# Performance work log

Hardware: AMD Instinct MI355X
Metric: run time of the kernel (lower is better)

The kernel has to match this reference:

```python
import jax, jax.numpy as jnp
import numpy as np

N = 50000        # nodes
E = 200000       # edges
D_IN = 128       # dim_input
D_E = 32         # dim_edge_features
D_H = 256        # dim_hidden
D_OUT = 256      # dim_output
N_LAYERS = 3
N_FRAG = 10000
N_GRAPH = 2000
BN_EPS = 1e-5
GINE_EPS = 0.0   # eps buffer, train_eps=False

_LAYER_DIMS = [(D_IN, D_H), (D_H, D_H), (D_H, D_OUT)]  # (node in, node out) per layer


def setup_inputs() -> dict:
    key = jax.random.key(0)
    ks = iter(jax.random.split(key, 64))
    inp = {}
    inp['x'] = jax.random.normal(next(ks), (N, D_IN), dtype=jnp.float32)
    inp['edge_attr'] = jax.random.normal(next(ks), (E, D_E), dtype=jnp.float32)
    inp['edge_index'] = jax.random.randint(next(ks), (2, E), 0, N, dtype=jnp.int64)
    inp['frag_batch'] = jnp.sort(jax.random.randint(next(ks), (N,), 0, N_FRAG, dtype=jnp.int64))
    inp['graph_batch'] = jnp.sort(jax.random.randint(next(ks), (N,), 0, N_GRAPH, dtype=jnp.int64))
    for i, (din, dout) in enumerate(_LAYER_DIMS):
        fin = din + D_E  # MLP input = node feat + edge feat (post-concat message)
        inp[f'w1_{i}'] = jax.random.normal(next(ks), (fin, D_H), dtype=jnp.float32) / np.sqrt(fin)
        inp[f'b1_{i}'] = jnp.zeros((D_H,), dtype=jnp.float32)
        inp[f'w2_{i}'] = jax.random.normal(next(ks), (D_H, dout), dtype=jnp.float32) / np.sqrt(D_H)
        inp[f'b2_{i}'] = jnp.zeros((dout,), dtype=jnp.float32)
        inp[f'g_{i}'] = jnp.ones((dout,), dtype=jnp.float32)     # BN weight
        inp[f'beta_{i}'] = jnp.zeros((dout,), dtype=jnp.float32)  # BN bias
    return inp


def _gine_layer(x, edge_attr, src, dst, w1, b1, w2, b2, g, beta):
    # message: relu(concat(x_j, e_ji)) gathered along edges  -> [E, din+De]
    m = jax.nn.relu(jnp.concatenate([x[src], edge_attr], axis=-1))
    # aggregate: scatter-add into target nodes -> [N, din+De]
    agg = jax.ops.segment_sum(m, dst, num_segments=N)
    # (1+eps)*x residual on the node-feature slice
    agg = agg.at[:, : x.shape[1]].add((1.0 + GINE_EPS) * x)
    # h_Theta MLP: Linear -> ReLU -> Linear
    h = jnp.dot(jax.nn.relu(jnp.dot(agg, w1) + b1), w2) + b2
    # ReLU then BatchNorm1d(track_running_stats=False): batch stats, biased var
    h = jax.nn.relu(h)
    mu = h.mean(axis=0)
    var = h.var(axis=0)
    return g * (h - mu) * jax.lax.rsqrt(var + BN_EPS) + beta


def _sqrt_pool(h, batch, num_segments):
    # nodes_per_graph, broadcast back per-node, sqrt-normalize, then add-pool
    cnt = jax.ops.segment_sum(jnp.ones((h.shape[0],), h.dtype), batch, num_segments=num_segments)
    inv_sqrt = jax.lax.rsqrt(jnp.maximum(cnt, 1.0))[batch]  # [N]
    return jax.ops.segment_sum(h * inv_sqrt[:, None], batch, num_segments=num_segments)


def reference(x, edge_attr, edge_index, frag_batch, graph_batch,
              w1_0, b1_0, w2_0, b2_0, g_0, beta_0,
              w1_1, b1_1, w2_1, b2_1, g_1, beta_1,
              w1_2, b1_2, w2_2, b2_2, g_2, beta_2):
    src, dst = edge_index[0], edge_index[1]
    params = [(w1_0, b1_0, w2_0, b2_0, g_0, beta_0),
              (w1_1, b1_1, w2_1, b2_1, g_1, beta_1),
              (w1_2, b1_2, w2_2, b2_2, g_2, beta_2)]
    h = x
    for p in params:
        h = _gine_layer(h, edge_attr, src, dst, *p)
    frag_out = _sqrt_pool(h, frag_batch, N_FRAG)    # [N_FRAG, D_OUT]
    graph_out = _sqrt_pool(h, graph_batch, N_GRAPH)  # [N_GRAPH, D_OUT]
    return (frag_out, graph_out)
```

## Files before the change

kernel.cpp:

```cpp
#include <hip/hip_runtime.h>

#define N_NODES 50000
#define N_EDGES 200000
#define DE 32
#define N_FRAG 10000
#define N_GRAPH 2000
#define BN_SLOTS 32
#define KSTR 296

typedef _Float16 f16x8 __attribute__((ext_vector_type(8)));
typedef _Float16 f16x4 __attribute__((ext_vector_type(4)));
typedef __attribute__((ext_vector_type(4))) float f32x4;

__device__ __forceinline__ float4 ld4(const float* p) { return *(const float4*)p; }
__device__ __forceinline__ float4 ld4(const _Float16* p) {
    f16x4 h = *(const f16x4*)p;
    float4 v; v.x = (float)h[0]; v.y = (float)h[1]; v.z = (float)h[2]; v.w = (float)h[3];
    return v;
}
__device__ __forceinline__ void st4h(_Float16* p, float4 v) {
    f16x4 h = {(_Float16)v.x, (_Float16)v.y, (_Float16)v.z, (_Float16)v.w};
    *(f16x4*)p = h;
}

__global__ __launch_bounds__(256)
void block_sum_kernel(const int* __restrict__ deg, int* __restrict__ bsum) {
    int i = blockIdx.x * 256 + threadIdx.x;
    int v = (i < N_NODES) ? deg[i] : 0;
#pragma unroll
    for (int o = 1; o < 64; o <<= 1) v += __shfl_xor(v, o);
    __shared__ int wsum[4];
    if ((threadIdx.x & 63) == 0) wsum[threadIdx.x >> 6] = v;
    __syncthreads();
    if (threadIdx.x == 0) bsum[blockIdx.x] = wsum[0] + wsum[1] + wsum[2] + wsum[3];
}

__global__ __launch_bounds__(256)
void top_scan_kernel(int* __restrict__ bsum, int nb) {
    __shared__ int s[256];
    int t = threadIdx.x;
    s[t] = (t < nb) ? bsum[t] : 0;
    __syncthreads();
    for (int o = 1; o < 256; o <<= 1) {
        int v = s[t];
        int a = (t >= o) ? s[t - o] : 0;
        __syncthreads();
        s[t] = v + a;
        __syncthreads();
    }
    if (t < nb) bsum[t] = (t > 0) ? s[t - 1] : 0;
}

__global__ __launch_bounds__(256)
void final_scan_kernel(const int* __restrict__ deg, const int* __restrict__ bsum,
                       int* __restrict__ ptr) {
    __shared__ int s[256];
    int i = blockIdx.x * 256 + threadIdx.x;
    int t = threadIdx.x;
    int v = (i < N_NODES) ? deg[i] : 0;
    s[t] = v;
    __syncthreads();
    for (int o = 1; o < 256; o <<= 1) {
        int x = s[t];
        int a = (t >= o) ? s[t - o] : 0;
        __syncthreads();
        s[t] = x + a;
        __syncthreads();
    }
    int incl = s[t];
    int base = bsum[blockIdx.x];
    if (i < N_NODES) ptr[i] = base + incl - v;
    if (i == N_NODES - 1) ptr[N_NODES] = base + incl;
}

__global__ __launch_bounds__(256)
void fill_csr_kernel(const int* __restrict__ ei, const int* __restrict__ row_ptr,
                     int* __restrict__ fill, int* __restrict__ csr_src,
                     int* __restrict__ csr_eid) {
    int e = blockIdx.x * 256 + threadIdx.x;
    if (e >= N_EDGES) return;
    int dst = ei[N_EDGES + e];
    int pos = row_ptr[dst] + atomicAdd(&fill[dst], 1);
    csr_src[pos] = ei[e];
    csr_eid[pos] = e;
}

struct PrepArgs {
    const float* W[6];
    _Float16* BS[6];
    int base[7];
    int nb_bs;
    const int* ei;
    int* deg;
    int nb_deg;
    const int* fb; const int* gb;
    int* frag_ptr; int* graph_ptr;
    int nb_seg;
    const float* x;
    _Float16* y0;
};

__global__ __launch_bounds__(256)
void prep1_kernel(PrepArgs a) {
    int b = blockIdx.x;
    const int t = threadIdx.x;
    if (b < a.nb_bs) {
        int id = b * 256 + t;
        if (id < a.base[6]) {
            int seg = 0;
#pragma unroll
            for (int i = 1; i < 6; ++i) seg += (id >= a.base[i]);
            int lid = id - a.base[seg];
            int j  = lid & 7;
            int l  = (lid >> 3) & 63;
            int cg = (lid >> 9) & 15;
            int kt = lid >> 13;
            int col = cg * 16 + (l & 15);
            int k   = kt * 32 + (l >> 4) * 8 + j;
            a.BS[seg][lid] = (_Float16)a.W[seg][(size_t)k * 256 + col];
        }
        return;
    }
    b -= a.nb_bs;
    if (b < a.nb_deg) {
        int e = b * 256 + t;
        if (e < N_EDGES) atomicAdd(&a.deg[a.ei[N_EDGES + e]], 1);
        return;
    }
    b -= a.nb_deg;
    if (b < a.nb_seg) {
        int id = b * 256 + t;
        const int* batch;
        int* ptr;
        int s;
        if (id <= N_FRAG) { batch = a.fb; ptr = a.frag_ptr; s = id; }
        else if (id <= N_FRAG + 1 + N_GRAPH) { batch = a.gb; ptr = a.graph_ptr; s = id - (N_FRAG + 1); }
        else return;
        int lo = 0, hi = N_NODES;
        while (lo < hi) {
            int mid = (lo + hi) >> 1;
            if (batch[mid] < s) lo = mid + 1; else hi = mid;
        }
        ptr[s] = lo;
        return;
    }
    b -= a.nb_seg;
    size_t i = ((size_t)b * 256 + t) * 4;
    if (i < (size_t)N_NODES * 128) {
        float4 v = ld4(a.x + i);
        f16x4 o = {(_Float16)fmaxf(v.x, 0.f), (_Float16)fmaxf(v.y, 0.f),
                   (_Float16)fmaxf(v.z, 0.f), (_Float16)fmaxf(v.w, 0.f)};
        *(f16x4*)(a.y0 + i) = o;
    }
}

__global__ __launch_bounds__(256)
void bnfin_relu16_kernel(const float* __restrict__ slots,
                         const float* __restrict__ g, const float* __restrict__ beta,
                         const _Float16* __restrict__ h, _Float16* __restrict__ y,
                         float* __restrict__ scale_out, float* __restrict__ shift_out) {
    __shared__ float ssc[256], ssh[256];
    const int t = threadIdx.x;
    {
        float s = 0.f, q = 0.f;
        for (int k = 0; k < BN_SLOTS; ++k) {
            s += slots[(size_t)k * 512 + t];
            q += slots[(size_t)k * 512 + 256 + t];
        }
        float mu = s * (1.0f / N_NODES);
        float var = q * (1.0f / N_NODES) - mu * mu;
        float rstd = rsqrtf(var + 1e-5f);
        float sc = g[t] * rstd;
        float sh = beta[t] - mu * sc;
        ssc[t] = sc; ssh[t] = sh;
        if (blockIdx.x == 0) { scale_out[t] = sc; shift_out[t] = sh; }
    }
    __syncthreads();
    const size_t total = (size_t)N_NODES * 256 / 8;
    for (size_t idx = (size_t)blockIdx.x * 256 + t; idx < total;
         idx += (size_t)gridDim.x * 256) {
        size_t i = idx * 8;
        int col = (int)(i & 255);
        f16x8 v = *(const f16x8*)(h + i);
        f16x8 o;
#pragma unroll
        for (int k2 = 0; k2 < 8; ++k2)
            o[k2] = (_Float16)fmaxf(fmaf((float)v[k2], ssc[col + k2], ssh[col + k2]), 0.f);
        *(f16x8*)(y + i) = o;
    }
}

template <bool BNIN, typename T, int NC>
__global__ __launch_bounds__(512, 4)
void fused_mlp_kernel(const T* __restrict__ X, const _Float16* __restrict__ Yg,
                      const int* __restrict__ row_ptr, const int* __restrict__ csr_src,
                      const int* __restrict__ csr_eid, const float* __restrict__ ea,
                      float* __restrict__ agg_e,
                      const float* __restrict__ bnsc, const float* __restrict__ bnsh,
                      const _Float16* __restrict__ B1, const float* __restrict__ bias1,
                      const _Float16* __restrict__ B2, const float* __restrict__ bias2,
                      _Float16* __restrict__ C, float* __restrict__ bnslot) {
    constexpr int DIN  = NC * 32;
    constexpr int K1   = DIN + 32;
    constexpr int NKT1 = K1 / 32;
    constexpr int CPT  = DIN / 8;
    constexpr int NV   = CPT / 8;
    __shared__ __align__(16) _Float16 sBuf[64 * KSTR];
    const int t = threadIdx.x;
    const int l = t & 63;
    const int w = t >> 6;
    const int lr = l & 15;
    const int lq = l >> 4;
    const int row0 = blockIdx.x << 6;
    const int cb = w << 5;

    {
        const int r = t >> 3, j = t & 7;
        const int jc = j << 3;
        const int gr = row0 + r;
        if (gr < N_NODES) {
            f16x8 acc16[NV];
#pragma unroll
            for (int c = 0; c < NV; ++c) acc16[c] = (f16x8){0, 0, 0, 0, 0, 0, 0, 0};
            float4 eacc = {0.f, 0.f, 0.f, 0.f};
            const int beg = row_ptr[gr], end = row_ptr[gr + 1];
            for (int e = beg; e < end; ++e) {
                const _Float16* sp = Yg + (size_t)csr_src[e] * DIN + jc;
#pragma unroll
                for (int c = 0; c < NV; ++c) acc16[c] += *(const f16x8*)(sp + c * 64);
                if (!BNIN) {
                    float4 ev = *(const float4*)(ea + (size_t)csr_eid[e] * DE + (j << 2));
                    eacc.x += fmaxf(ev.x, 0.f);
                    eacc.y += fmaxf(ev.y, 0.f);
                    eacc.z += fmaxf(ev.z, 0.f);
                    eacc.w += fmaxf(ev.w, 0.f);
                }
            }
            const T* xp = X + (size_t)gr * DIN + jc;
#pragma unroll
            for (int c = 0; c < NV; ++c) {
                float4 v0f = ld4(xp + c * 64);
                float4 v1f = ld4(xp + c * 64 + 4);
                if (BNIN) {
                    float4 sa = *(const float4*)(bnsc + c * 64 + jc);
                    float4 sb = *(const float4*)(bnsc + c * 64 + jc + 4);
                    float4 ta = *(const float4*)(bnsh + c * 64 + jc);
                    float4 tb = *(const float4*)(bnsh + c * 64 + jc + 4);
                    v0f.x = fmaf(v0f.x, sa.x, ta.x);
                    v0f.y = fmaf(v0f.y, sa.y, ta.y);
                    v0f.z = fmaf(v0f.z, sa.z, ta.z);
                    v0f.w = fmaf(v0f.w, sa.w, ta.w);
                    v1f.x = fmaf(v1f.x, sb.x, tb.x);
                    v1f.y = fmaf(v1f.y, sb.y, tb.y);
                    v1f.z = fmaf(v1f.z, sb.z, tb.z);
                    v1f.w = fmaf(v1f.w, sb.w, tb.w);
                }
                f16x8 o;
                o[0] = (_Float16)(v0f.x + (float)acc16[c][0]);
                o[1] = (_Float16)(v0f.y + (float)acc16[c][1]);
                o[2] = (_Float16)(v0f.z + (float)acc16[c][2]);
                o[3] = (_Float16)(v0f.w + (float)acc16[c][3]);
                o[4] = (_Float16)(v1f.x + (float)acc16[c][4]);
                o[5] = (_Float16)(v1f.y + (float)acc16[c][5]);
                o[6] = (_Float16)(v1f.z + (float)acc16[c][6]);
                o[7] = (_Float16)(v1f.w + (float)acc16[c][7]);
                *(f16x8*)&sBuf[r * KSTR + c * 64 + jc] = o;
            }
            if (!BNIN) {
                *(float4*)(agg_e + (size_t)gr * DE + (j << 2)) = eacc;
                st4h(&sBuf[r * KSTR + DIN + (j << 2)], eacc);
            } else {
                float4 ev = *(const float4*)(agg_e + (size_t)gr * DE + (j << 2));
                st4h(&sBuf[r * KSTR + DIN + (j << 2)], ev);
            }
        } else {
            f16x8 z8 = {0, 0, 0, 0, 0, 0, 0, 0};
#pragma unroll
            for (int c = 0; c < NV; ++c)
                *(f16x8*)&sBuf[r * KSTR + c * 64 + jc] = z8;
            f16x4 z4 = {0, 0, 0, 0};
            *(f16x4*)&sBuf[r * KSTR + DIN + (j << 2)] = z4;
        }
    }
    __syncthreads();

    f32x4 acc1[4][2];
#pragma unroll
    for (int mt = 0; mt < 4; ++mt)
#pragma unroll
        for (int nt = 0; nt < 2; ++nt) acc1[mt][nt] = (f32x4){0.f, 0.f, 0.f, 0.f};
#pragma unroll
    for (int kt = 0; kt < NKT1; ++kt) {
        f16x8 af[4], bf[2];
#pragma unroll
        for (int mt = 0; mt < 4; ++mt)
            af[mt] = *(const f16x8*)&sBuf[(mt * 16 + lr) * KSTR + (kt << 5) + (lq << 3)];
        const size_t bb = ((size_t)(kt * 16 + (w << 1))) * 512 + (l << 3);
#pragma unroll
        for (int nt = 0; nt < 2; ++nt)
            bf[nt] = *(const f16x8*)(B1 + bb + nt * 512);
#pragma unroll
        for (int mt = 0; mt < 4; ++mt)
#pragma unroll
            for (int nt = 0; nt < 2; ++nt)
                acc1[mt][nt] = __builtin_amdgcn_mfma_f32_16x16x32_f16(
                    af[mt], bf[nt], acc1[mt][nt], 0, 0, 0);
    }
    __syncthreads();

#pragma unroll
    for (int nt = 0; nt < 2; ++nt) {
        int col = cb + nt * 16 + lr;
        float bv = bias1[col];
#pragma unroll
        for (int mt = 0; mt < 4; ++mt)
#pragma unroll
            for (int i = 0; i < 4; ++i) {
                int rr = mt * 16 + lq * 4 + i;
                sBuf[rr * KSTR + col] = (_Float16)fmaxf(acc1[mt][nt][i] + bv, 0.f);
            }
    }
    __syncthreads();

    f32x4 acc2[4][2];
#pragma unroll
    for (int mt = 0; mt < 4; ++mt)
#pragma unroll
        for (int nt = 0; nt < 2; ++nt) acc2[mt][nt] = (f32x4){0.f, 0.f, 0.f, 0.f};
#pragma unroll
    for (int kt = 0; kt < 8; ++kt) {
        f16x8 af[4], bf[2];
#pragma unroll
        for (int mt = 0; mt < 4; ++mt)
            af[mt] = *(const f16x8*)&sBuf[(mt * 16 + lr) * KSTR + (kt << 5) + (lq << 3)];
        const size_t bb = ((size_t)(kt * 16 + (w << 1))) * 512 + (l << 3);
#pragma unroll
        for (int nt = 0; nt < 2; ++nt)
            bf[nt] = *(const f16x8*)(B2 + bb + nt * 512);
#pragma unroll
        for (int mt = 0; mt < 4; ++mt)
#pragma unroll
            for (int nt = 0; nt < 2; ++nt)
                acc2[mt][nt] = __builtin_amdgcn_mfma_f32_16x16x32_f16(
                    af[mt], bf[nt], acc2[mt][nt], 0, 0, 0);
    }
    __syncthreads();

    float* slot = bnslot + (size_t)(blockIdx.x & (BN_SLOTS - 1)) * 512;
#pragma unroll
    for (int nt = 0; nt < 2; ++nt) {
        int col = cb + nt * 16 + lr;
        float bv = bias2[col];
        float s = 0.f, qq = 0.f;
#pragma unroll
        for (int mt = 0; mt < 4; ++mt)
#pragma unroll
            for (int i = 0; i < 4; ++i) {
                int rr = mt * 16 + lq * 4 + i;
                float o = fmaxf(acc2[mt][nt][i] + bv, 0.f);
                sBuf[rr * KSTR + col] = (_Float16)o;
                if (row0 + rr < N_NODES) { s += o; qq += o * o; }
            }
        s += __shfl_xor(s, 16); s += __shfl_xor(s, 32);
        qq += __shfl_xor(qq, 16); qq += __shfl_xor(qq, 32);
        if (lq == 0) {
            atomicAdd(&slot[col], s);
            atomicAdd(&slot[256 + col], qq);
        }
    }
    __syncthreads();

#pragma unroll
    for (int k = 0; k < 4; ++k) {
        int rr  = (t >> 5) + k * 16;
        int col = (t & 31) * 8;
        int row = row0 + rr;
        if (row < N_NODES) {
            f16x8 v = *(const f16x8*)&sBuf[rr * KSTR + col];
            *(f16x8*)(C + (size_t)row * 256 + col) = v;
        }
    }
}

__global__ __launch_bounds__(256)
void pool_both_kernel(const _Float16* __restrict__ h,
                      const int* __restrict__ frag_ptr, const int* __restrict__ graph_ptr,
                      const float* __restrict__ slots,
                      const float* __restrict__ g2, const float* __restrict__ beta2,
                      float* __restrict__ out) {
    __shared__ float ssc[256], ssh[256];
    const int t = threadIdx.x;
    {
        float s = 0.f, q = 0.f;
        for (int k = 0; k < BN_SLOTS; ++k) {
            s += slots[(size_t)k * 512 + t];
            q += slots[(size_t)k * 512 + 256 + t];
        }
        float mu = s * (1.0f / N_NODES);
        float var = q * (1.0f / N_NODES) - mu * mu;
        float rstd = rsqrtf(var + 1e-5f);
        float sc = g2[t] * rstd;
        ssc[t] = sc;
        ssh[t] = beta2[t] - mu * sc;
    }
    __syncthreads();
    const int NFB = (N_FRAG + 3) / 4;
    int b = blockIdx.x;
    const int* ptr; float* o; int nseg; int sb;
    if (b < NFB) { ptr = frag_ptr; o = out; nseg = N_FRAG; sb = b * 4; }
    else { ptr = graph_ptr; o = out + (size_t)N_FRAG * 256; nseg = N_GRAPH; sb = (b - NFB) * 4; }
    int g = t >> 6;
    int j = t & 63;
    int s = sb + g;
    if (s >= nseg) return;
    int beg = ptr[s], end = ptr[s + 1];
    int col = j << 2;
    float4 sc = *(const float4*)(ssc + col);
    float4 sh = *(const float4*)(ssh + col);
    float4 acc = {0.f, 0.f, 0.f, 0.f};
    for (int i = beg; i < end; ++i) {
        float4 v = ld4(h + (size_t)i * 256 + col);
        acc.x += fmaf(v.x, sc.x, sh.x);
        acc.y += fmaf(v.y, sc.y, sh.y);
        acc.z += fmaf(v.z, sc.z, sh.z);
        acc.w += fmaf(v.w, sc.w, sh.w);
    }
    float w = rsqrtf(fmaxf((float)(end - beg), 1.0f));
    float4 ov = {acc.x * w, acc.y * w, acc.z * w, acc.w * w};
    *(float4*)(o + (size_t)s * 256 + col) = ov;
}

extern "C" void kernel_launch(void* const* d_in, const int* in_sizes, int n_in,
                              void* d_out, int out_size, void* d_ws, size_t ws_size,
                              hipStream_t stream) {
    const float* x  = (const float*)d_in[0];
    const float* ea = (const float*)d_in[1];
    const int*   ei = (const int*)d_in[2];
    const int*   fb = (const int*)d_in[3];
    const int*   gb = (const int*)d_in[4];
    const float* W1[3]   = {(const float*)d_in[5],  (const float*)d_in[11], (const float*)d_in[17]};
    const float* B1[3]   = {(const float*)d_in[6],  (const float*)d_in[12], (const float*)d_in[18]};
    const float* W2[3]   = {(const float*)d_in[7],  (const float*)d_in[13], (const float*)d_in[19]};
    const float* B2[3]   = {(const float*)d_in[8],  (const float*)d_in[14], (const float*)d_in[20]};
    const float* G[3]    = {(const float*)d_in[9],  (const float*)d_in[15], (const float*)d_in[21]};
    const float* BETA[3] = {(const float*)d_in[10], (const float*)d_in[16], (const float*)d_in[22]};

    const int FIN[3] = {160, 288, 288};
    const int NBLK = (N_NODES + 255) / 256;

    float* ws = (float*)d_ws;
    size_t off = 0;
    _Float16* bufA = (_Float16*)(ws + off); off += (size_t)N_NODES * 128;
    _Float16* bufB = (_Float16*)(ws + off); off += (size_t)N_NODES * 128;
    _Float16* ybuf = (_Float16*)(ws + off); off += (size_t)N_NODES * 128;
    float* agg_e = ws + off; off += (size_t)N_NODES * DE;
    float* bnss  = ws + off; off += 3 * 512;
    float* bnslots = ws + off; off += (size_t)3 * BN_SLOTS * 512;
    _Float16* w1f[3]; _Float16* w2f[3];
    {
        _Float16* sw = (_Float16*)(ws + off);
        _Float16* sw0 = sw;
        for (int l = 0; l < 3; ++l) { w1f[l] = sw; sw += 256 * FIN[l]; }
        for (int l = 0; l < 3; ++l) { w2f[l] = sw; sw += 256 * 256; }
        off += (size_t)(sw - sw0 + 1) / 2;
    }
    int* iw      = (int*)(ws + off);
    int* row_ptr = iw;                     iw += N_NODES + 1;
    int* deg     = iw;                     iw += N_NODES;
    int* fill    = iw;                     iw += N_NODES;
    int* csr_src = iw;                     iw += N_EDGES;
    int* csr_eid = iw;                     iw += N_EDGES;
    int* frag_ptr = iw;                    iw += N_FRAG + 1;
    int* graph_ptr = iw;                   iw += N_GRAPH + 1;
    int* bsum    = iw;                     iw += NBLK;

    hipMemsetAsync(deg, 0, 2 * N_NODES * sizeof(int), stream);
    hipMemsetAsync(bnslots, 0, (size_t)3 * BN_SLOTS * 512 * sizeof(float), stream);

    {
        PrepArgs a;
        a.W[0] = W1[0]; a.W[1] = W1[1]; a.W[2] = W1[2];
        a.W[3] = W2[0]; a.W[4] = W2[1]; a.W[5] = W2[2];
        a.BS[0] = w1f[0]; a.BS[1] = w1f[1]; a.BS[2] = w1f[2];
        a.BS[3] = w2f[0]; a.BS[4] = w2f[1]; a.BS[5] = w2f[2];
        int Ks[6] = {FIN[0], FIN[1], FIN[2], 256, 256, 256};
        int cum = 0;
        for (int i = 0; i < 6; ++i) { a.base[i] = cum; cum += Ks[i] * 256; }
        a.base[6] = cum;
        a.nb_bs  = (cum + 255) / 256;
        a.ei = ei; a.deg = deg;
        a.nb_deg = (N_EDGES + 255) / 256;
        a.fb = fb; a.gb = gb; a.frag_ptr = frag_ptr; a.graph_ptr = graph_ptr;
        a.nb_seg = (N_FRAG + N_GRAPH + 2 + 255) / 256;
        a.x = x; a.y0 = ybuf;
        int nb_relu = (N_NODES * 128 / 4 + 255) / 256;
        prep1_kernel<<<a.nb_bs + a.nb_deg + a.nb_seg + nb_relu, 256, 0, stream>>>(a);
    }

    block_sum_kernel<<<NBLK, 256, 0, stream>>>(deg, bsum);
    top_scan_kernel<<<1, 256, 0, stream>>>(bsum, NBLK);
    final_scan_kernel<<<NBLK, 256, 0, stream>>>(deg, bsum, row_ptr);
    fill_csr_kernel<<<(N_EDGES + 255) / 256, 256, 0, stream>>>(ei, row_ptr, fill, csr_src, csr_eid);

    const int nblk_mlp = (N_NODES + 63) / 64;
    fused_mlp_kernel<false, float, 4><<<nblk_mlp, 512, 0, stream>>>(
        x, ybuf, row_ptr, csr_src, csr_eid, ea, agg_e, nullptr, nullptr,
        w1f[0], B1[0], w2f[0], B2[0], bufA, bnslots);

    bnfin_relu16_kernel<<<512, 256, 0, stream>>>(
        bnslots, G[0], BETA[0], bufA, ybuf, bnss, bnss + 256);
    fused_mlp_kernel<true, _Float16, 8><<<nblk_mlp, 512, 0, stream>>>(
        bufA, ybuf, row_ptr, csr_src, nullptr, nullptr, agg_e, bnss, bnss + 256,
        w1f[1], B1[1], w2f[1], B2[1], bufB, bnslots + (size_t)1 * BN_SLOTS * 512);

    bnfin_relu16_kernel<<<512, 256, 0, stream>>>(
        bnslots + (size_t)1 * BN_SLOTS * 512, G[1], BETA[1], bufB, ybuf,
        bnss + 512, bnss + 768);
    fused_mlp_kernel<true, _Float16, 8><<<nblk_mlp, 512, 0, stream>>>(
        bufB, ybuf, row_ptr, csr_src, nullptr, nullptr, agg_e, bnss + 512, bnss + 768,
        w1f[2], B1[2], w2f[2], B2[2], bufA, bnslots + (size_t)2 * BN_SLOTS * 512);

    const int NFB = (N_FRAG + 3) / 4, NGB = (N_GRAPH + 3) / 4;
    pool_both_kernel<<<NFB + NGB, 256, 0, stream>>>(
        bufA, frag_ptr, graph_ptr, bnslots + (size_t)2 * BN_SLOTS * 512,
        G[2], BETA[2], (float*)d_out);
}
```

Before: 335.2 us.

## Fuse BN-finalize+ReLU into MLP gather and merge CSR scan/fill into one kernel

Removes the standalone BN-finalize/ReLU kernels: each fused MLP block now recomputes scale/shift from the BN slots and applies BN+ReLU on the fly to gathered neighbor rows in fp16. The three-kernel degree scan plus CSR fill are merged into one kernel using decoupled look-back and a grid-wide spin barrier, and the bnslots memset is folded into the prep kernel. This cuts several launches and a full read/write pass over the hidden activations, at the cost of redundant per-block BN reductions, extra fp16 math per gathered edge, and a grid barrier that relies on all 196 blocks being co-resident.

Result: slower. 364.9 us (+8.9%).

```diff
diff --git a/kernel.cpp b/kernel.cpp
--- a/kernel.cpp
+++ b/kernel.cpp
@@ -7,6 +7,7 @@
 #define N_GRAPH 2000
 #define BN_SLOTS 32
 #define KSTR 296
+#define NSCAN ((N_NODES + 255) / 256)
 
 typedef _Float16 f16x8 __attribute__((ext_vector_type(8)));
 typedef _Float16 f16x4 __attribute__((ext_vector_type(4)));
@@ -21,68 +22,6 @@
 __device__ __forceinline__ void st4h(_Float16* p, float4 v) {
     f16x4 h = {(_Float16)v.x, (_Float16)v.y, (_Float16)v.z, (_Float16)v.w};
     *(f16x4*)p = h;
-}
-
-__global__ __launch_bounds__(256)
-void block_sum_kernel(const int* __restrict__ deg, int* __restrict__ bsum) {
-    int i = blockIdx.x * 256 + threadIdx.x;
-    int v = (i < N_NODES) ? deg[i] : 0;
-#pragma unroll
-    for (int o = 1; o < 64; o <<= 1) v += __shfl_xor(v, o);
-    __shared__ int wsum[4];
-    if ((threadIdx.x & 63) == 0) wsum[threadIdx.x >> 6] = v;
-    __syncthreads();
-    if (threadIdx.x == 0) bsum[blockIdx.x] = wsum[0] + wsum[1] + wsum[2] + wsum[3];
-}
-
-__global__ __launch_bounds__(256)
-void top_scan_kernel(int* __restrict__ bsum, int nb) {
-    __shared__ int s[256];
-    int t = threadIdx.x;
-    s[t] = (t < nb) ? bsum[t] : 0;
-    __syncthreads();
-    for (int o = 1; o < 256; o <<= 1) {
-        int v = s[t];
-        int a = (t >= o) ? s[t - o] : 0;
-        __syncthreads();
-        s[t] = v + a;
-        __syncthreads();
-    }
-    if (t < nb) bsum[t] = (t > 0) ? s[t - 1] : 0;
-}
-
-__global__ __launch_bounds__(256)
-void final_scan_kernel(const int* __restrict__ deg, const int* __restrict__ bsum,
-                       int* __restrict__ ptr) {
-    __shared__ int s[256];
-    int i = blockIdx.x * 256 + threadIdx.x;
-    int t = threadIdx.x;
-    int v = (i < N_NODES) ? deg[i] : 0;
-    s[t] = v;
-    __syncthreads();
-    for (int o = 1; o < 256; o <<= 1) {
-        int x = s[t];
-        int a = (t >= o) ? s[t - o] : 0;
-        __syncthreads();
-        s[t] = x + a;
-        __syncthreads();
-    }
-    int incl = s[t];
-    int base = bsum[blockIdx.x];
-    if (i < N_NODES) ptr[i] = base + incl - v;
-    if (i == N_NODES - 1) ptr[N_NODES] = base + incl;
-}
-
-__global__ __launch_bounds__(256)
-void fill_csr_kernel(const int* __restrict__ ei, const int* __restrict__ row_ptr,
-                     int* __restrict__ fill, int* __restrict__ csr_src,
-                     int* __restrict__ csr_eid) {
-    int e = blockIdx.x * 256 + threadIdx.x;
-    if (e >= N_EDGES) return;
-    int dst = ei[N_EDGES + e];
-    int pos = row_ptr[dst] + atomicAdd(&fill[dst], 1);
-    csr_src[pos] = ei[e];
-    csr_eid[pos] = e;
 }
 
 struct PrepArgs {
@@ -98,6 +37,8 @@
     int nb_seg;
     const float* x;
     _Float16* y0;
+    int nb_relu;
+    float* bnslots;
 };
 
 __global__ __launch_bounds__(256)
@@ -145,48 +86,84 @@
         return;
     }
     b -= a.nb_seg;
-    size_t i = ((size_t)b * 256 + t) * 4;
-    if (i < (size_t)N_NODES * 128) {
-        float4 v = ld4(a.x + i);
-        f16x4 o = {(_Float16)fmaxf(v.x, 0.f), (_Float16)fmaxf(v.y, 0.f),
-                   (_Float16)fmaxf(v.z, 0.f), (_Float16)fmaxf(v.w, 0.f)};
-        *(f16x4*)(a.y0 + i) = o;
-    }
+    if (b < a.nb_relu) {
+        size_t i = ((size_t)b * 256 + t) * 4;
+        if (i < (size_t)N_NODES * 128) {
+            float4 v = ld4(a.x + i);
+            f16x4 o = {(_Float16)fmaxf(v.x, 0.f), (_Float16)fmaxf(v.y, 0.f),
+                       (_Float16)fmaxf(v.z, 0.f), (_Float16)fmaxf(v.w, 0.f)};
+            *(f16x4*)(a.y0 + i) = o;
+        }
+        return;
+    }
+    b -= a.nb_relu;
+    int zi = b * 256 + t;
+    if (zi < 3 * BN_SLOTS * 512) a.bnslots[zi] = 0.f;
 }
 
 __global__ __launch_bounds__(256)
-void bnfin_relu16_kernel(const float* __restrict__ slots,
-                         const float* __restrict__ g, const float* __restrict__ beta,
-                         const _Float16* __restrict__ h, _Float16* __restrict__ y,
-                         float* __restrict__ scale_out, float* __restrict__ shift_out) {
-    __shared__ float ssc[256], ssh[256];
-    const int t = threadIdx.x;
-    {
-        float s = 0.f, q = 0.f;
-        for (int k = 0; k < BN_SLOTS; ++k) {
-            s += slots[(size_t)k * 512 + t];
-            q += slots[(size_t)k * 512 + 256 + t];
-        }
-        float mu = s * (1.0f / N_NODES);
-        float var = q * (1.0f / N_NODES) - mu * mu;
-        float rstd = rsqrtf(var + 1e-5f);
-        float sc = g[t] * rstd;
-        float sh = beta[t] - mu * sc;
-        ssc[t] = sc; ssh[t] = sh;
-        if (blockIdx.x == 0) { scale_out[t] = sc; shift_out[t] = sh; }
-    }
-    __syncthreads();
-    const size_t total = (size_t)N_NODES * 256 / 8;
-    for (size_t idx = (size_t)blockIdx.x * 256 + t; idx < total;
-         idx += (size_t)gridDim.x * 256) {
-        size_t i = idx * 8;
-        int col = (int)(i & 255);
-        f16x8 v = *(const f16x8*)(h + i);
-        f16x8 o;
-#pragma unroll
-        for (int k2 = 0; k2 < 8; ++k2)
-            o[k2] = (_Float16)fmaxf(fmaf((float)v[k2], ssc[col + k2], ssh[col + k2]), 0.f);
-        *(f16x8*)(y + i) = o;
+void scan_fill_kernel(const int* __restrict__ deg, const int* __restrict__ ei,
+                      int* __restrict__ row_ptr, int* __restrict__ fill,
+                      int* __restrict__ csr_src, int* __restrict__ csr_eid,
+                      int* __restrict__ agg, int* __restrict__ incl,
+                      int* __restrict__ state, int* __restrict__ done) {
+    __shared__ int s[256];
+    __shared__ int sexcl;
+    const int b = blockIdx.x, t = threadIdx.x;
+    const int i = b * 256 + t;
+    int v = (i < N_NODES) ? deg[i] : 0;
+    s[t] = v;
+    __syncthreads();
+    for (int o = 1; o < 256; o <<= 1) {
+        int x = s[t];
+        int a = (t >= o) ? s[t - o] : 0;
+        __syncthreads();
+        s[t] = x + a;
+        __syncthreads();
+    }
+    int total = s[255];
+    if (t == 0) {
+        if (b == 0) {
+            incl[0] = total;
+            __threadfence();
+            atomicExch(&state[0], 2);
+            sexcl = 0;
+        } else {
+            agg[b] = total;
+            __threadfence();
+            atomicExch(&state[b], 1);
+            int excl = 0;
+            int p = b - 1;
+            while (p >= 0) {
+                int st;
+                do { st = atomicAdd(&state[p], 0); } while (st == 0);
+                if (st == 2) { excl += atomicAdd(&incl[p], 0); break; }
+                excl += atomicAdd(&agg[p], 0);
+                --p;
+            }
+            incl[b] = excl + total;
+            __threadfence();
+            atomicExch(&state[b], 2);
+            sexcl = excl;
+        }
+    }
+    __syncthreads();
+    int base = sexcl;
+    if (i < N_NODES) row_ptr[i] = base + s[t] - v;
+    if (i == N_NODES - 1) row_ptr[N_NODES] = base + s[t];
+    __threadfence();
+    __syncthreads();
+    if (t == 0) {
+        atomicAdd(done, 1);
+        while (atomicAdd(done, 0) < (int)gridDim.x) {}
+    }
+    __syncthreads();
+    __threadfence();
+    for (int e = b * 256 + t; e < N_EDGES; e += gridDim.x * 256) {
+        int dst = ei[N_EDGES + e];
+        int pos = row_ptr[dst] + atomicAdd(&fill[dst], 1);
+        csr_src[pos] = ei[e];
+        csr_eid[pos] = e;
     }
 }
 
@@ -196,7 +173,8 @@
                       const int* __restrict__ row_ptr, const int* __restrict__ csr_src,
                       const int* __restrict__ csr_eid, const float* __restrict__ ea,
                       float* __restrict__ agg_e,
-                      const float* __restrict__ bnsc, const float* __restrict__ bnsh,
+                      const float* __restrict__ prev_slots,
+                      const float* __restrict__ prev_g, const float* __restrict__ prev_beta,
                       const _Float16* __restrict__ B1, const float* __restrict__ bias1,
                       const _Float16* __restrict__ B2, const float* __restrict__ bias2,
                       _Float16* __restrict__ C, float* __restrict__ bnslot) {
@@ -206,6 +184,7 @@
     constexpr int CPT  = DIN / 8;
     constexpr int NV   = CPT / 8;
     __shared__ __align__(16) _Float16 sBuf[64 * KSTR];
+    __shared__ float ssc[256], ssh[256];
     const int t = threadIdx.x;
     const int l = t & 63;
     const int w = t >> 6;
@@ -214,10 +193,38 @@
     const int row0 = blockIdx.x << 6;
     const int cb = w << 5;
 
+    if (BNIN) {
+        if (t < 256) {
+            float s = 0.f, q = 0.f;
+            for (int k = 0; k < BN_SLOTS; ++k) {
+                s += prev_slots[(size_t)k * 512 + t];
+                q += prev_slots[(size_t)k * 512 + 256 + t];
+            }
+            float mu = s * (1.0f / N_NODES);
+            float var = q * (1.0f / N_NODES) - mu * mu;
+            float rstd = rsqrtf(var + 1e-5f);
+            float sc = prev_g[t] * rstd;
+            ssc[t] = sc;
+            ssh[t] = prev_beta[t] - mu * sc;
+        }
+        __syncthreads();
+    }
+
     {
         const int r = t >> 3, j = t & 7;
         const int jc = j << 3;
         const int gr = row0 + r;
+        const _Float16* nbp = BNIN ? (const _Float16*)(const void*)X : Yg;
+        f16x8 sc16[NV], sh16[NV];
+        if (BNIN) {
+#pragma unroll
+            for (int c = 0; c < NV; ++c)
+#pragma unroll
+                for (int k = 0; k < 8; ++k) {
+                    sc16[c][k] = (_Float16)ssc[c * 64 + jc + k];
+                    sh16[c][k] = (_Float16)ssh[c * 64 + jc + k];
+                }
+        }
         if (gr < N_NODES) {
             f16x8 acc16[NV];
 #pragma unroll
@@ -225,9 +232,20 @@
             float4 eacc = {0.f, 0.f, 0.f, 0.f};
             const int beg = row_ptr[gr], end = row_ptr[gr + 1];
             for (int e = beg; e < end; ++e) {
-                const _Float16* sp = Yg + (size_t)csr_src[e] * DIN + jc;
-#pragma unroll
-                for (int c = 0; c < NV; ++c) acc16[c] += *(const f16x8*)(sp + c * 64);
+                const _Float16* sp = nbp + (size_t)csr_src[e] * DIN + jc;
+#pragma unroll
+                for (int c = 0; c < NV; ++c) {
+                    f16x8 v = *(const f16x8*)(sp + c * 64);
+                    if (BNIN) {
+                        f16x8 yy = v * sc16[c] + sh16[c];
+#pragma unroll
+                        for (int k = 0; k < 8; ++k)
+                            yy[k] = (yy[k] > (_Float16)0.f) ? yy[k] : (_Float16)0.f;
+                        acc16[c] += yy;
+                    } else {
+                        acc16[c] += v;
+                    }
+                }
                 if (!BNIN) {
                     float4 ev = *(const float4*)(ea + (size_t)csr_eid[e] * DE + (j << 2));
                     eacc.x += fmaxf(ev.x, 0.f);
@@ -242,10 +260,10 @@
                 float4 v0f = ld4(xp + c * 64);
                 float4 v1f = ld4(xp + c * 64 + 4);
                 if (BNIN) {
-                    float4 sa = *(const float4*)(bnsc + c * 64 + jc);
-                    float4 sb = *(const float4*)(bnsc + c * 64 + jc + 4);
-                    float4 ta = *(const float4*)(bnsh + c * 64 + jc);
-                    float4 tb = *(const float4*)(bnsh + c * 64 + jc + 4);
+                    float4 sa = *(const float4*)(ssc + c * 64 + jc);
+                    float4 sb = *(const float4*)(ssc + c * 64 + jc + 4);
+                    float4 ta = *(const float4*)(ssh + c * 64 + jc);
+                    float4 tb = *(const float4*)(ssh + c * 64 + jc + 4);
                     v0f.x = fmaf(v0f.x, sa.x, ta.x);
                     v0f.y = fmaf(v0f.y, sa.y, ta.y);
                     v0f.z = fmaf(v0f.z, sa.z, ta.z);
@@ -446,7 +464,6 @@
     const float* BETA[3] = {(const float*)d_in[10], (const float*)d_in[16], (const float*)d_in[22]};
 
     const int FIN[3] = {160, 288, 288};
-    const int NBLK = (N_NODES + 255) / 256;
 
     float* ws = (float*)d_ws;
     size_t off = 0;
@@ -454,7 +471,6 @@
     _Float16* bufB = (_Float16*)(ws + off); off += (size_t)N_NODES * 128;
     _Float16* ybuf = (_Float16*)(ws + off); off += (size_t)N_NODES * 128;
     float* agg_e = ws + off; off += (size_t)N_NODES * DE;
-    float* bnss  = ws + off; off += 3 * 512;
     float* bnslots = ws + off; off += (size_t)3 * BN_SLOTS * 512;
     _Float16* w1f[3]; _Float16* w2f[3];
     {
@@ -465,17 +481,19 @@
         off += (size_t)(sw - sw0 + 1) / 2;
     }
     int* iw      = (int*)(ws + off);
-    int* row_ptr = iw;                     iw += N_NODES + 1;
-    int* deg     = iw;                     iw += N_NODES;
-    int* fill    = iw;                     iw += N_NODES;
-    int* csr_src = iw;                     iw += N_EDGES;
-    int* csr_eid = iw;                     iw += N_EDGES;
+    int* deg      = iw;                    iw += N_NODES;
+    int* fill     = iw;                    iw += N_NODES;
+    int* sc_agg   = iw;                    iw += NSCAN;
+    int* sc_incl  = iw;                    iw += NSCAN;
+    int* sc_state = iw;                    iw += NSCAN;
+    int* sc_done  = iw;                    iw += 1;
+    int* row_ptr  = iw;                    iw += N_NODES + 1;
+    int* csr_src  = iw;                    iw += N_EDGES;
+    int* csr_eid  = iw;                    iw += N_EDGES;
     int* frag_ptr = iw;                    iw += N_FRAG + 1;
     int* graph_ptr = iw;                   iw += N_GRAPH + 1;
-    int* bsum    = iw;                     iw += NBLK;
-
-    hipMemsetAsync(deg, 0, 2 * N_NODES * sizeof(int), stream);
-    hipMemsetAsync(bnslots, 0, (size_t)3 * BN_SLOTS * 512 * sizeof(float), stream);
+
+    hipMemsetAsync(deg, 0, (size_t)(2 * N_NODES + 3 * NSCAN + 1) * sizeof(int), stream);
 
     {
         PrepArgs a;
@@ -493,31 +511,31 @@
         a.fb = fb; a.gb = gb; a.frag_ptr = frag_ptr; a.graph_ptr = graph_ptr;
         a.nb_seg = (N_FRAG + N_GRAPH + 2 + 255) / 256;
         a.x = x; a.y0 = ybuf;
-        int nb_relu = (N_NODES * 128 / 4 + 255) / 256;
-        prep1_kernel<<<a.nb_bs + a.nb_deg + a.nb_seg + nb_relu, 256, 0, stream>>>(a);
-    }
-
-    block_sum_kernel<<<NBLK, 256, 0, stream>>>(deg, bsum);
-    top_scan_kernel<<<1, 256, 0, stream>>>(bsum, NBLK);
-    final_scan_kernel<<<NBLK, 256, 0, stream>>>(deg, bsum, row_ptr);
-    fill_csr_kernel<<<(N_EDGES + 255) / 256, 256, 0, stream>>>(ei, row_ptr, fill, csr_src, csr_eid);
+        a.nb_relu = (N_NODES * 128 / 4 + 255) / 256;
+        a.bnslots = bnslots;
+        int nb_zero = (3 * BN_SLOTS * 512 + 255) / 256;
+        prep1_kernel<<<a.nb_bs + a.nb_deg + a.nb_seg + a.nb_relu + nb_zero,
+                       256, 0, stream>>>(a);
+    }
+
+    scan_fill_kernel<<<NSCAN, 256, 0, stream>>>(
+        deg, ei, row_ptr, fill, csr_src, csr_eid,
+        sc_agg, sc_incl, sc_state, sc_done);
 
     const int nblk_mlp = (N_NODES + 63) / 64;
     fused_mlp_kernel<false, float, 4><<<nblk_mlp, 512, 0, stream>>>(
-        x, ybuf, row_ptr, csr_src, csr_eid, ea, agg_e, nullptr, nullptr,
+        x, ybuf, row_ptr, csr_src, csr_eid, ea, agg_e,
+        nullptr, nullptr, nullptr,
         w1f[0], B1[0], w2f[0], B2[0], bufA, bnslots);
 
-    bnfin_relu16_kernel<<<512, 256, 0, stream>>>(
-        bnslots, G[0], BETA[0], bufA, ybuf, bnss, bnss + 256);
     fused_mlp_kernel<true, _Float16, 8><<<nblk_mlp, 512, 0, stream>>>(
-        bufA, ybuf, row_ptr, csr_src, nullptr, nullptr, agg_e, bnss, bnss + 256,
+        bufA, nullptr, row_ptr, csr_src, nullptr, nullptr, agg_e,
+        bnslots, G[0], BETA[0],
         w1f[1], B1[1], w2f[1], B2[1], bufB, bnslots + (size_t)1 * BN_SLOTS * 512);
 
-    bnfin_relu16_kernel<<<512, 256, 0, stream>>>(
-        bnslots + (size_t)1 * BN_SLOTS * 512, G[1], BETA[1], bufB, ybuf,
-        bnss + 512, bnss + 768);
     fused_mlp_kernel<true, _Float16, 8><<<nblk_mlp, 512, 0, stream>>>(
-        bufB, ybuf, row_ptr, csr_src, nullptr, nullptr, agg_e, bnss + 512, bnss + 768,
+        bufB, nullptr, row_ptr, csr_src, nullptr, nullptr, agg_e,
+        bnslots + (size_t)1 * BN_SLOTS * 512, G[1], BETA[1],
         w1f[2], B1[2], w2f[2], B2[2], bufA, bnslots + (size_t)2 * BN_SLOTS * 512);
 
     const int NFB = (N_FRAG + 3) / 4, NGB = (N_GRAPH + 3) / 4;
```
